# Performance work log

Measured on AMD Instinct MI355X. Metric: run time of the kernel, lower is better.

Reference implementation:

```python
import jax, jax.numpy as jnp
import numpy as np

B = 16384        # batch
N_IN = 784       # n_input_neurons
D = 64           # n_neurons_per_hidd_bank
N_LAYERS = 6     # layers of hidden banks
BANKS = 6        # banks per layer (n_hidd_banks = 36)
N_OUT = 10       # n_output_neurons
EPS = 1e-5       # BatchNorm1d eps


def setup_inputs() -> dict:
    key = jax.random.key(0)
    ks = jax.random.split(key, 8)
    x = jax.random.normal(ks[0], (B, N_IN), dtype=jnp.float32)
    gamma_in = jnp.ones((N_IN,), jnp.float32)
    beta_in = jnp.zeros((N_IN,), jnp.float32)
    # input2hidden Linear(N_IN -> D) for each of the 6 input banks (layer 0)
    W_in = jax.random.normal(ks[1], (BANKS, D, N_IN), jnp.float32) * 0.03
    b_in = jax.random.normal(ks[2], (BANKS, D), jnp.float32) * 0.03
    # per-edge gate Linear(D -> 1, no bias) and data Linear(D -> D, bias)
    # indexed [layer, source_bank, target_bank, ...]
    Wg = jax.random.normal(ks[3], (N_LAYERS - 1, BANKS, BANKS, D), jnp.float32) * 0.1
    Wd = jax.random.normal(ks[4], (N_LAYERS - 1, BANKS, BANKS, D, D), jnp.float32) * 0.1
    bd = jax.random.normal(ks[5], (N_LAYERS - 1, BANKS, BANKS, D), jnp.float32) * 0.1
    # per-bank BatchNorm1d(D) affine params, [layer, bank, D]
    gamma_h = jnp.ones((N_LAYERS, BANKS, D), jnp.float32)
    beta_h = jnp.zeros((N_LAYERS, BANKS, D), jnp.float32)
    # hidden2output Linear(D -> N_OUT, no bias) for the 6 output banks (last layer)
    W_out = jax.random.normal(ks[6], (BANKS, N_OUT, D), jnp.float32) * 0.1
    return dict(x=x, gamma_in=gamma_in, beta_in=beta_in, W_in=W_in, b_in=b_in,
                Wg=Wg, Wd=Wd, bd=bd, gamma_h=gamma_h, beta_h=beta_h, W_out=W_out)


def _bn(x, g, b):
    # training-mode BatchNorm1d: normalize over batch axis 0, biased variance
    mu = jnp.mean(x, axis=0)
    var = jnp.mean((x - mu) ** 2, axis=0)
    return g * (x - mu) * jax.lax.rsqrt(var + EPS) + b


def reference(x, gamma_in, beta_in, W_in, b_in, Wg, Wd, bd, gamma_h, beta_h, W_out):
    xb = _bn(x, gamma_in, beta_in)                                  # [B, N_IN]
    # input banks: relu(input2hidden(x)); then (as targets with no sources)
    # relu (idempotent) + BatchNorm, matching the target loop in torch
    acts = jax.nn.relu(jnp.einsum('bn,kdn->bkd', xb, W_in) + b_in)  # [B, 6, D]
    acts = _bn(jax.nn.relu(acts), gamma_h[0], beta_h[0])
    total_gate = jnp.zeros((x.shape[0], 1), x.dtype)                # sum of [B,1] gate acts
    for l in range(N_LAYERS - 1):
        # gate: hardtanh(Linear(D->1), 0, 1) per edge (s,t)
        gate = jnp.clip(jnp.einsum('bsd,std->bst', acts, Wg[l]), 0.0, 1.0)  # [B,6,6]
        # data: Linear(D->D) per edge
        data = jnp.einsum('bsd,sted->bste', acts, Wd[l]) + bd[l]            # [B,6,6,D]
        pre = jnp.einsum('bst,bste->bte', gate, data)                       # sum over sources
        total_gate = total_gate + jnp.sum(gate, axis=(1, 2))[:, None]
        acts = _bn(jax.nn.relu(pre), gamma_h[l + 1], beta_h[l + 1])         # [B,6,D]
    # output banks = last layer banks; sum of Linear(D->N_OUT, no bias)
    output = jnp.einsum('bkd,kod->bo', acts, W_out)                         # [B, N_OUT]
    return output, total_gate
```

## Files before the change

### kernel.cpp

```cpp
#include <hip/hip_runtime.h>
#include <hip/hip_bf16.h>

#define BATCH   16384
#define NIN     784
#define NH      384
#define NLAYERS 6
#define NOUT    10
#define EPS_BN  1e-5f
#define LOSCALE 2048.0f
#define LOINV   (1.0f/2048.0f)
#define NPART   128
#define PSTRIDE 1024

typedef __attribute__((ext_vector_type(8))) _Float16 f16x8;
typedef __attribute__((ext_vector_type(4))) _Float16 f16x4;
typedef __attribute__((ext_vector_type(4))) float f32x4;

__global__ __launch_bounds__(256) void stats_partial(
        const float* __restrict__ src, int C, int applyRelu,
        float* __restrict__ psum, float* __restrict__ psq) {
    int c = blockIdx.x * 256 + threadIdx.x;
    if (c >= C) return;
    int r0 = blockIdx.y * (BATCH / NPART);
    float s = 0.f, q = 0.f;
    for (int r = r0; r < r0 + BATCH / NPART; ++r) {
        float v = src[(size_t)r * C + c];
        if (applyRelu) v = fmaxf(v, 0.f);
        s += v; q += v * v;
    }
    psum[blockIdx.y * PSTRIDE + c] = s;
    psq [blockIdx.y * PSTRIDE + c] = q;
}

__global__ __launch_bounds__(256) void stats_finalize(
        const float* __restrict__ psum, const float* __restrict__ psq, int C,
        const float* __restrict__ gamma, const float* __restrict__ beta,
        float* __restrict__ a_out, float* __restrict__ c_out) {
    int c = blockIdx.x * 256 + threadIdx.x;
    if (c >= C) return;
    float s = 0.f, q = 0.f;
    for (int i = 0; i < NPART; ++i) { s += psum[i * PSTRIDE + c]; q += psq[i * PSTRIDE + c]; }
    const float invB = 1.f / (float)BATCH;
    float mu  = s * invB;
    float var = q * invB - mu * mu;
    float rs  = rsqrtf(var + EPS_BN);
    float g   = gamma[c];
    a_out[c] = g * rs;
    c_out[c] = beta[c] - g * mu * rs;
}

__global__ __launch_bounds__(256) void scale_win_hl(
        const float* __restrict__ W_in, const float* __restrict__ a,
        _Float16* __restrict__ whi, _Float16* __restrict__ wlo) {
    int i = blockIdx.x * 256 + threadIdx.x;
    if (i >= NH * NIN / 4) return;
    int n = (i * 4) % NIN;
    float4 wv = ((const float4*)W_in)[i];
    float v[4] = { wv.x * a[n], wv.y * a[n + 1], wv.z * a[n + 2], wv.w * a[n + 3] };
    f16x4 h4, l4;
    #pragma unroll
    for (int j = 0; j < 4; ++j) {
        _Float16 h = (_Float16)v[j];
        h4[j] = h;
        l4[j] = (_Float16)((v[j] - (float)h) * LOSCALE);
    }
    *(f16x4*)(whi + (size_t)i * 4) = h4;
    *(f16x4*)(wlo + (size_t)i * 4) = l4;
}

__global__ __launch_bounds__(256) void conv_hl(
        const float* __restrict__ src, _Float16* __restrict__ hi,
        _Float16* __restrict__ lo, int n4) {
    int i = blockIdx.x * 256 + threadIdx.x;
    if (i >= n4) return;
    float4 wv = ((const float4*)src)[i];
    float v[4] = { wv.x, wv.y, wv.z, wv.w };
    f16x4 h4, l4;
    #pragma unroll
    for (int j = 0; j < 4; ++j) {
        _Float16 h = (_Float16)v[j];
        h4[j] = h;
        l4[j] = (_Float16)((v[j] - (float)h) * LOSCALE);
    }
    *(f16x4*)(hi + (size_t)i * 4) = h4;
    *(f16x4*)(lo + (size_t)i * 4) = l4;
}

__global__ __launch_bounds__(256) void prep_wg(
        const float* __restrict__ Wg, _Float16* __restrict__ hi,
        _Float16* __restrict__ lo) {
    int idx = blockIdx.x * 256 + threadIdx.x;
    if (idx >= 5 * 48 * 384) return;
    int l = idx / (48 * 384);
    int r = idx % (48 * 384);
    int st = r / 384, k = r % 384;
    float v = 0.f;
    if (st < 36 && (k >> 6) == st / 6)
        v = Wg[l * 36 * 64 + st * 64 + (k & 63)];
    _Float16 h = (_Float16)v;
    hi[idx] = h;
    lo[idx] = (_Float16)((v - (float)h) * LOSCALE);
}

__global__ __launch_bounds__(256) void prep_wout(
        const float* __restrict__ W_out, _Float16* __restrict__ hi,
        _Float16* __restrict__ lo) {
    int idx = blockIdx.x * 256 + threadIdx.x;
    if (idx >= 16 * 384) return;
    int o = idx / 384, k = idx % 384;
    float v = 0.f;
    if (o < NOUT) v = W_out[((k >> 6) * NOUT + o) * 64 + (k & 63)];
    _Float16 h = (_Float16)v;
    hi[idx] = h;
    lo[idx] = (_Float16)((v - (float)h) * LOSCALE);
}

__global__ __launch_bounds__(64) void bias_in(
        const float* __restrict__ W_in, const float* __restrict__ b_in,
        const float* __restrict__ cvec, float* __restrict__ bp) {
    int j = blockIdx.x;
    int lane = threadIdx.x;
    float s = 0.f;
    for (int n = lane; n < NIN; n += 64) s += cvec[n] * W_in[j * NIN + n];
    #pragma unroll
    for (int m = 1; m < 64; m <<= 1) s += __shfl_xor(s, m, 64);
    if (lane == 0) bp[j] = b_in[j] + s;
}

__global__ __launch_bounds__(256, 2) void gemm_in_mfma(
        const float* __restrict__ X, const _Float16* __restrict__ Wphi,
        const _Float16* __restrict__ Wplo, const float* __restrict__ bp,
        float* __restrict__ pre) {
    int tid = threadIdx.x;
    int w = tid >> 6, l = tid & 63, lr = l & 15, lq = l >> 4;
    int b0 = blockIdx.x * 128 + w * 32;
    int n0 = blockIdx.y * 64;
    const float* xrow0 = X + (size_t)(b0 + lr) * NIN;
    const float* xrow1 = X + (size_t)(b0 + 16 + lr) * NIN;
    f32x4 acc[4][2], acr[4][2];
    #pragma unroll
    for (int ct = 0; ct < 4; ++ct)
        #pragma unroll
        for (int bt = 0; bt < 2; ++bt)
            #pragma unroll
            for (int r = 0; r < 4; ++r) { acc[ct][bt][r] = 0.f; acr[ct][bt][r] = 0.f; }
    for (int kc = 0; kc < 24; ++kc) {
        int k0 = kc * 32 + lq * 8;
        f16x8 ahi[2], alo[2];
        {
            float4 x0 = *(const float4*)(xrow0 + k0);
            float4 x1 = *(const float4*)(xrow0 + k0 + 4);
            float xv[8] = { x0.x, x0.y, x0.z, x0.w, x1.x, x1.y, x1.z, x1.w };
            #pragma unroll
            for (int j = 0; j < 8; ++j) {
                _Float16 h = (_Float16)xv[j];
                ahi[0][j] = h;
                alo[0][j] = (_Float16)((xv[j] - (float)h) * LOSCALE);
            }
            float4 y0 = *(const float4*)(xrow1 + k0);
            float4 y1 = *(const float4*)(xrow1 + k0 + 4);
            float yv[8] = { y0.x, y0.y, y0.z, y0.w, y1.x, y1.y, y1.z, y1.w };
            #pragma unroll
            for (int j = 0; j < 8; ++j) {
                _Float16 h = (_Float16)yv[j];
                ahi[1][j] = h;
                alo[1][j] = (_Float16)((yv[j] - (float)h) * LOSCALE);
            }
        }
        #pragma unroll
        for (int ct = 0; ct < 4; ++ct) {
            size_t off = (size_t)(n0 + ct * 16 + lr) * NIN + k0;
            f16x8 bhi = *(const f16x8*)(Wphi + off);
            f16x8 blo = *(const f16x8*)(Wplo + off);
            #pragma unroll
            for (int bt = 0; bt < 2; ++bt) {
                acc[ct][bt] = __builtin_amdgcn_mfma_f32_16x16x32_f16(ahi[bt], bhi, acc[ct][bt], 0, 0, 0);
                acr[ct][bt] = __builtin_amdgcn_mfma_f32_16x16x32_f16(ahi[bt], blo, acr[ct][bt], 0, 0, 0);
                acr[ct][bt] = __builtin_amdgcn_mfma_f32_16x16x32_f16(alo[bt], bhi, acr[ct][bt], 0, 0, 0);
            }
        }
    }
    {
        f16x8 ahi[2], alo[2];
        #pragma unroll
        for (int bt = 0; bt < 2; ++bt)
            #pragma unroll
            for (int j = 0; j < 8; ++j) { ahi[bt][j] = (_Float16)0.f; alo[bt][j] = (_Float16)0.f; }
        if (lq < 2) {
            const float* xr[2] = { xrow0, xrow1 };
            #pragma unroll
            for (int bt = 0; bt < 2; ++bt) {
                float4 x0 = *(const float4*)(xr[bt] + 768 + lq * 8);
                float4 x1 = *(const float4*)(xr[bt] + 768 + lq * 8 + 4);
                float xv[8] = { x0.x, x0.y, x0.z, x0.w, x1.x, x1.y, x1.z, x1.w };
                #pragma unroll
                for (int j = 0; j < 8; ++j) {
                    _Float16 h = (_Float16)xv[j];
                    ahi[bt][j] = h;
                    alo[bt][j] = (_Float16)((xv[j] - (float)h) * LOSCALE);
                }
            }
        }
        #pragma unroll
        for (int ct = 0; ct < 4; ++ct) {
            f16x8 bhi, blo;
            #pragma unroll
            for (int j = 0; j < 8; ++j) { bhi[j] = (_Float16)0.f; blo[j] = (_Float16)0.f; }
            if (lq < 2) {
                size_t off = (size_t)(n0 + ct * 16 + lr) * NIN + 768 + lq * 8;
                bhi = *(const f16x8*)(Wphi + off);
                blo = *(const f16x8*)(Wplo + off);
            }
            #pragma unroll
            for (int bt = 0; bt < 2; ++bt) {
                acc[ct][bt] = __builtin_amdgcn_mfma_f32_16x16x32_f16(ahi[bt], bhi, acc[ct][bt], 0, 0, 0);
                acr[ct][bt] = __builtin_amdgcn_mfma_f32_16x16x32_f16(ahi[bt], blo, acr[ct][bt], 0, 0, 0);
                acr[ct][bt] = __builtin_amdgcn_mfma_f32_16x16x32_f16(alo[bt], bhi, acr[ct][bt], 0, 0, 0);
            }
        }
    }
    #pragma unroll
    for (int ct = 0; ct < 4; ++ct) {
        int n = n0 + ct * 16 + lr;
        float bias = bp[n];
        #pragma unroll
        for (int bt = 0; bt < 2; ++bt) {
            int brow = b0 + bt * 16 + lq * 4;
            #pragma unroll
            for (int r = 0; r < 4; ++r)
                pre[(size_t)(brow + r) * NH + n] = acc[ct][bt][r] + LOINV * acr[ct][bt][r] + bias;
        }
    }
}

__global__ __launch_bounds__(256, 2) void normgate_mfma(
        const float* __restrict__ pre, const float* __restrict__ a,
        const float* __restrict__ c, const _Float16* __restrict__ WgHi,
        const _Float16* __restrict__ WgLo, _Float16* __restrict__ aHi,
        _Float16* __restrict__ aLo, float* __restrict__ gateT,
        float* __restrict__ tg, int firstLayer) {
    __shared__ float red[24][3][64];
    int tid = threadIdx.x;
    int kw = tid >> 6, l = tid & 63, lr = l & 15, lq = l >> 4;
    int b = blockIdx.x * 16 + lr;
    const float* prow = pre + (size_t)b * NH;
    f32x4 acc[3], acr[3];
    #pragma unroll
    for (int rt = 0; rt < 3; ++rt)
        #pragma unroll
        for (int r = 0; r < 4; ++r) { acc[rt][r] = 0.f; acr[rt][r] = 0.f; }
    #pragma unroll
    for (int kk = 0; kk < 3; ++kk) {
        int k0 = (kw * 3 + kk) * 32 + lq * 8;
        float4 v0 = *(const float4*)(prow + k0);
        float4 v1 = *(const float4*)(prow + k0 + 4);
        float4 a0 = *(const float4*)(a + k0);
        float4 a1 = *(const float4*)(a + k0 + 4);
        float4 c0 = *(const float4*)(c + k0);
        float4 c1 = *(const float4*)(c + k0 + 4);
        float y[8] = {
            a0.x * fmaxf(v0.x, 0.f) + c0.x, a0.y * fmaxf(v0.y, 0.f) + c0.y,
            a0.z * fmaxf(v0.z, 0.f) + c0.z, a0.w * fmaxf(v0.w, 0.f) + c0.w,
            a1.x * fmaxf(v1.x, 0.f) + c1.x, a1.y * fmaxf(v1.y, 0.f) + c1.y,
            a1.z * fmaxf(v1.z, 0.f) + c1.z, a1.w * fmaxf(v1.w, 0.f) + c1.w };
        f16x8 bhi, blo;
        #pragma unroll
        for (int j = 0; j < 8; ++j) {
            _Float16 h = (_Float16)y[j];
            bhi[j] = h;
            blo[j] = (_Float16)((y[j] - (float)h) * LOSCALE);
        }
        *(f16x8*)(aHi + (size_t)b * NH + k0) = bhi;
        *(f16x8*)(aLo + (size_t)b * NH + k0) = blo;
        #pragma unroll
        for (int rt = 0; rt < 3; ++rt) {
            size_t off = (size_t)(rt * 16 + lr) * NH + k0;
            f16x8 whi = *(const f16x8*)(WgHi + off);
            f16x8 wlo = *(const f16x8*)(WgLo + off);
            acc[rt] = __builtin_amdgcn_mfma_f32_16x16x32_f16(whi, bhi, acc[rt], 0, 0, 0);
            acr[rt] = __builtin_amdgcn_mfma_f32_16x16x32_f16(whi, blo, acr[rt], 0, 0, 0);
            acr[rt] = __builtin_amdgcn_mfma_f32_16x16x32_f16(wlo, bhi, acr[rt], 0, 0, 0);
        }
    }
    if (kw > 0) {
        #pragma unroll
        for (int rt = 0; rt < 3; ++rt)
            #pragma unroll
            for (int r = 0; r < 4; ++r) {
                red[rt * 4 + r][kw - 1][l]      = acc[rt][r];
                red[12 + rt * 4 + r][kw - 1][l] = acr[rt][r];
            }
    }
    __syncthreads();
    if (kw == 0) {
        #pragma unroll
        for (int rt = 0; rt < 3; ++rt)
            #pragma unroll
            for (int r = 0; r < 4; ++r) {
                #pragma unroll
                for (int wv = 0; wv < 3; ++wv) {
                    acc[rt][r] += red[rt * 4 + r][wv][l];
                    acr[rt][r] += red[12 + rt * 4 + r][wv][l];
                }
            }
        float gsum = 0.f;
        #pragma unroll
        for (int rt = 0; rt < 3; ++rt)
            #pragma unroll
            for (int r = 0; r < 4; ++r) {
                int st = rt * 16 + lq * 4 + r;
                if (st < 36) {
                    float p = acc[rt][r] + LOINV * acr[rt][r];
                    float g = fminf(fmaxf(p, 0.f), 1.f);
                    gateT[(size_t)st * BATCH + b] = g;
                    gsum += g;
                }
            }
        gsum += __shfl_xor(gsum, 16, 64);
        gsum += __shfl_xor(gsum, 32, 64);
        if (lq == 0) tg[b] = (firstLayer ? 0.f : tg[b]) + gsum;
    }
}

__global__ __launch_bounds__(256, 2) void layer_data_mfma(
        const _Float16* __restrict__ aHi, const _Float16* __restrict__ aLo,
        const float* __restrict__ gateT, const _Float16* __restrict__ Wdhi,
        const _Float16* __restrict__ Wdlo, const float* __restrict__ bd_l,
        float* __restrict__ pre) {
    int tid = threadIdx.x;
    int w = tid >> 6, l = tid & 63, lr = l & 15, lq = l >> 4;
    int b0 = blockIdx.x * 32;
    int t0 = blockIdx.y * 3;
    int e0 = w * 16;
    f32x4 acc[3][2];
    #pragma unroll
    for (int t = 0; t < 3; ++t)
        #pragma unroll
        for (int ct = 0; ct < 2; ++ct)
            #pragma unroll
            for (int r = 0; r < 4; ++r) acc[t][ct][r] = 0.f;
    #pragma unroll 1
    for (int s = 0; s < 6; ++s) {
        f16x8 bhi[2][2], blo[2][2];
        #pragma unroll
        for (int ct = 0; ct < 2; ++ct) {
            size_t arow = (size_t)(b0 + ct * 16 + lr) * NH + s * 64 + lq * 8;
            #pragma unroll
            for (int ks = 0; ks < 2; ++ks) {
                bhi[ct][ks] = *(const f16x8*)(aHi + arow + ks * 32);
                blo[ct][ks] = *(const f16x8*)(aLo + arow + ks * 32);
            }
        }
        #pragma unroll
        for (int tt = 0; tt < 3; ++tt) {
            int t = t0 + tt;
            float g[2];
            #pragma unroll
            for (int ct = 0; ct < 2; ++ct)
                g[ct] = gateT[(size_t)(s * 6 + t) * BATCH + b0 + ct * 16 + lr];
            size_t wb = ((size_t)(s * 6 + t) * 64 + e0 + lr) * 64 + lq * 8;
            f16x8 ah0 = *(const f16x8*)(Wdhi + wb);
            f16x8 ah1 = *(const f16x8*)(Wdhi + wb + 32);
            f16x8 al0 = *(const f16x8*)(Wdlo + wb);
            f16x8 al1 = *(const f16x8*)(Wdlo + wb + 32);
            float bdv[4];
            #pragma unroll
            for (int r = 0; r < 4; ++r)
                bdv[r] = bd_l[(s * 6 + t) * 64 + e0 + lq * 4 + r];
            #pragma unroll
            for (int ct = 0; ct < 2; ++ct) {
                f32x4 ph, pc;
                #pragma unroll
                for (int r = 0; r < 4; ++r) { ph[r] = 0.f; pc[r] = 0.f; }
                ph = __builtin_amdgcn_mfma_f32_16x16x32_f16(ah0, bhi[ct][0], ph, 0, 0, 0);
                ph = __builtin_amdgcn_mfma_f32_16x16x32_f16(ah1, bhi[ct][1], ph, 0, 0, 0);
                pc = __builtin_amdgcn_mfma_f32_16x16x32_f16(ah0, blo[ct][0], pc, 0, 0, 0);
                pc = __builtin_amdgcn_mfma_f32_16x16x32_f16(ah1, blo[ct][1], pc, 0, 0, 0);
                pc = __builtin_amdgcn_mfma_f32_16x16x32_f16(al0, bhi[ct][0], pc, 0, 0, 0);
                pc = __builtin_amdgcn_mfma_f32_16x16x32_f16(al1, bhi[ct][1], pc, 0, 0, 0);
                #pragma unroll
                for (int r = 0; r < 4; ++r)
                    acc[tt][ct][r] += g[ct] * (ph[r] + LOINV * pc[r] + bdv[r]);
            }
        }
    }
    #pragma unroll
    for (int tt = 0; tt < 3; ++tt)
        #pragma unroll
        for (int ct = 0; ct < 2; ++ct)
            #pragma unroll
            for (int r = 0; r < 4; ++r)
                pre[(size_t)(b0 + ct * 16 + lr) * NH + (t0 + tt) * 64 + e0 + lq * 4 + r]
                    = acc[tt][ct][r];
}

__global__ __launch_bounds__(256, 2) void normout_mfma(
        const float* __restrict__ pre, const float* __restrict__ a,
        const float* __restrict__ c, const _Float16* __restrict__ OutHi,
        const _Float16* __restrict__ OutLo, const float* __restrict__ tg,
        float* __restrict__ dout) {
    __shared__ float red[8][3][64];
    int tid = threadIdx.x;
    int kw = tid >> 6, l = tid & 63, lr = l & 15, lq = l >> 4;
    int b = blockIdx.x * 16 + lr;
    const float* prow = pre + (size_t)b * NH;
    f32x4 acc, acr;
    #pragma unroll
    for (int r = 0; r < 4; ++r) { acc[r] = 0.f; acr[r] = 0.f; }
    #pragma unroll
    for (int kk = 0; kk < 3; ++kk) {
        int k0 = (kw * 3 + kk) * 32 + lq * 8;
        float4 v0 = *(const float4*)(prow + k0);
        float4 v1 = *(const float4*)(prow + k0 + 4);
        float4 a0 = *(const float4*)(a + k0);
        float4 a1 = *(const float4*)(a + k0 + 4);
        float4 c0 = *(const float4*)(c + k0);
        float4 c1 = *(const float4*)(c + k0 + 4);
        float y[8] = {
            a0.x * fmaxf(v0.x, 0.f) + c0.x, a0.y * fmaxf(v0.y, 0.f) + c0.y,
            a0.z * fmaxf(v0.z, 0.f) + c0.z, a0.w * fmaxf(v0.w, 0.f) + c0.w,
            a1.x * fmaxf(v1.x, 0.f) + c1.x, a1.y * fmaxf(v1.y, 0.f) + c1.y,
            a1.z * fmaxf(v1.z, 0.f) + c1.z, a1.w * fmaxf(v1.w, 0.f) + c1.w };
        f16x8 bhi, blo;
        #pragma unroll
        for (int j = 0; j < 8; ++j) {
            _Float16 h = (_Float16)y[j];
            bhi[j] = h;
            blo[j] = (_Float16)((y[j] - (float)h) * LOSCALE);
        }
        size_t off = (size_t)lr * NH + k0;
        f16x8 whi = *(const f16x8*)(OutHi + off);
        f16x8 wlo = *(const f16x8*)(OutLo + off);
        acc = __builtin_amdgcn_mfma_f32_16x16x32_f16(whi, bhi, acc, 0, 0, 0);
        acr = __builtin_amdgcn_mfma_f32_16x16x32_f16(whi, blo, acr, 0, 0, 0);
        acr = __builtin_amdgcn_mfma_f32_16x16x32_f16(wlo, bhi, acr, 0, 0, 0);
    }
    if (kw > 0) {
        #pragma unroll
        for (int r = 0; r < 4; ++r) {
            red[r][kw - 1][l]     = acc[r];
            red[4 + r][kw - 1][l] = acr[r];
        }
    }
    __syncthreads();
    if (kw == 0) {
        #pragma unroll
        for (int r = 0; r < 4; ++r)
            #pragma unroll
            for (int wv = 0; wv < 3; ++wv) {
                acc[r] += red[r][wv][l];
                acr[r] += red[4 + r][wv][l];
            }
        #pragma unroll
        for (int r = 0; r < 4; ++r) {
            int o = lq * 4 + r;
            if (o < NOUT)
                dout[(size_t)b * NOUT + o] = acc[r] + LOINV * acr[r];
        }
        if (lq == 0) dout[(size_t)BATCH * NOUT + b] = tg[b];
    }
}

extern "C" void kernel_launch(void* const* d_in, const int* in_sizes, int n_in,
                              void* d_out, int out_size, void* d_ws, size_t ws_size,
                              hipStream_t stream) {
    const float* x        = (const float*)d_in[0];
    const float* gamma_in = (const float*)d_in[1];
    const float* beta_in  = (const float*)d_in[2];
    const float* W_in     = (const float*)d_in[3];
    const float* b_in     = (const float*)d_in[4];
    const float* Wg       = (const float*)d_in[5];
    const float* Wd       = (const float*)d_in[6];
    const float* bd       = (const float*)d_in[7];
    const float* gamma_h  = (const float*)d_in[8];
    const float* beta_h   = (const float*)d_in[9];
    const float* W_out    = (const float*)d_in[10];
    float* dout = (float*)d_out;
    float* ws = (float*)d_ws;

    float* psum  = ws;
    float* psq   = ws + 131072;
    float* avec  = ws + 262144;
    float* cvec  = ws + 263168;
    float* bp    = ws + 264192;
    float* pre   = ws + 265216;
    _Float16* actsHi = (_Float16*)(ws + 6556672);
    _Float16* actsLo = (_Float16*)(ws + 9702400);
    float* gateT = ws + 12848128;
    float* tg    = ws + 13437952;
    _Float16* WpHi = (_Float16*)(ws + 13454336);
    _Float16* WpLo = (_Float16*)(ws + 13604864);
    _Float16* WdHiAll = (_Float16*)(ws + 13755392);
    _Float16* WdLoAll = (_Float16*)(ws + 14124032);
    _Float16* WgHiAll = (_Float16*)(ws + 14492672);
    _Float16* WgLoAll = (_Float16*)(ws + 14538752);
    _Float16* OutHi   = (_Float16*)(ws + 14584832);
    _Float16* OutLo   = (_Float16*)(ws + 14587904);

    dim3 blk(256);

    stats_partial<<<dim3(4, NPART), blk, 0, stream>>>(x, NIN, 0, psum, psq);
    stats_finalize<<<dim3(4), blk, 0, stream>>>(psum, psq, NIN, gamma_in, beta_in, avec, cvec);
    scale_win_hl<<<dim3((NH * NIN / 4 + 255) / 256), blk, 0, stream>>>(W_in, avec, WpHi, WpLo);
    bias_in<<<dim3(NH), dim3(64), 0, stream>>>(W_in, b_in, cvec, bp);
    conv_hl<<<dim3((5 * 36 * 4096 / 4 + 255) / 256), blk, 0, stream>>>(
            Wd, WdHiAll, WdLoAll, 5 * 36 * 4096 / 4);
    prep_wg<<<dim3((5 * 48 * 384 + 255) / 256), blk, 0, stream>>>(Wg, WgHiAll, WgLoAll);
    prep_wout<<<dim3((16 * 384 + 255) / 256), blk, 0, stream>>>(W_out, OutHi, OutLo);

    gemm_in_mfma<<<dim3(BATCH / 128, 6), blk, 0, stream>>>(x, WpHi, WpLo, bp, pre);

    for (int j = 0; j < NLAYERS; ++j) {
        stats_partial<<<dim3(2, NPART), blk, 0, stream>>>(pre, NH, 1, psum, psq);
        stats_finalize<<<dim3(2), blk, 0, stream>>>(psum, psq, NH,
                gamma_h + j * NH, beta_h + j * NH, avec, cvec);
        if (j < NLAYERS - 1) {
            int l = j;
            normgate_mfma<<<dim3(BATCH / 16), blk, 0, stream>>>(
                    pre, avec, cvec, WgHiAll + (size_t)l * 48 * 384,
                    WgLoAll + (size_t)l * 48 * 384, actsHi, actsLo, gateT, tg, l == 0);
            layer_data_mfma<<<dim3(BATCH / 32, 2), blk, 0, stream>>>(
                    actsHi, actsLo, gateT, WdHiAll + (size_t)l * 36 * 4096,
                    WdLoAll + (size_t)l * 36 * 4096, bd + (size_t)l * 36 * 64, pre);
        } else {
            normout_mfma<<<dim3(BATCH / 16), blk, 0, stream>>>(
                    pre, avec, cvec, OutHi, OutLo, tg, dout);
        }
    }
}
```

Baseline: 642.2 us.

## Split input GEMM K-dimension across waves with shared-memory reduction

```diff
diff --git a/kernel.cpp b/kernel.cpp
--- a/kernel.cpp
+++ b/kernel.cpp
@@ -131,9 +131,10 @@
         const float* __restrict__ X, const _Float16* __restrict__ Wphi,
         const _Float16* __restrict__ Wplo, const float* __restrict__ bp,
         float* __restrict__ pre) {
+    __shared__ float red[32][3][64];
     int tid = threadIdx.x;
-    int w = tid >> 6, l = tid & 63, lr = l & 15, lq = l >> 4;
-    int b0 = blockIdx.x * 128 + w * 32;
+    int kw = tid >> 6, l = tid & 63, lr = l & 15, lq = l >> 4;
+    int b0 = blockIdx.x * 32;
     int n0 = blockIdx.y * 64;
     const float* xrow0 = X + (size_t)(b0 + lr) * NIN;
     const float* xrow1 = X + (size_t)(b0 + 16 + lr) * NIN;
@@ -144,8 +145,8 @@
         for (int bt = 0; bt < 2; ++bt)
             #pragma unroll
             for (int r = 0; r < 4; ++r) { acc[ct][bt][r] = 0.f; acr[ct][bt][r] = 0.f; }
-    for (int kc = 0; kc < 24; ++kc) {
-        int k0 = kc * 32 + lq * 8;
+    for (int kk = 0; kk < 6; ++kk) {
+        int k0 = (kw * 6 + kk) * 32 + lq * 8;
         f16x8 ahi[2], alo[2];
         {
             float4 x0 = *(const float4*)(xrow0 + k0);
@@ -180,7 +181,7 @@
             }
         }
     }
-    {
+    if (kw == 3) {
         f16x8 ahi[2], alo[2];
         #pragma unroll
         for (int bt = 0; bt < 2; ++bt)
@@ -219,16 +220,34 @@
             }
         }
     }
-    #pragma unroll
-    for (int ct = 0; ct < 4; ++ct) {
-        int n = n0 + ct * 16 + lr;
-        float bias = bp[n];
-        #pragma unroll
-        for (int bt = 0; bt < 2; ++bt) {
-            int brow = b0 + bt * 16 + lq * 4;
-            #pragma unroll
-            for (int r = 0; r < 4; ++r)
-                pre[(size_t)(brow + r) * NH + n] = acc[ct][bt][r] + LOINV * acr[ct][bt][r] + bias;
+    if (kw > 0) {
+        #pragma unroll
+        for (int ct = 0; ct < 4; ++ct)
+            #pragma unroll
+            for (int bt = 0; bt < 2; ++bt)
+                #pragma unroll
+                for (int r = 0; r < 4; ++r)
+                    red[ct * 8 + bt * 4 + r][kw - 1][l]
+                        = acc[ct][bt][r] + LOINV * acr[ct][bt][r];
+    }
+    __syncthreads();
+    if (kw == 0) {
+        #pragma unroll
+        for (int ct = 0; ct < 4; ++ct) {
+            int n = n0 + ct * 16 + lr;
+            float bias = bp[n];
+            #pragma unroll
+            for (int bt = 0; bt < 2; ++bt) {
+                int brow = b0 + bt * 16 + lq * 4;
+                #pragma unroll
+                for (int r = 0; r < 4; ++r) {
+                    float v = acc[ct][bt][r] + LOINV * acr[ct][bt][r];
+                    #pragma unroll
+                    for (int wv = 0; wv < 3; ++wv)
+                        v += red[ct * 8 + bt * 4 + r][wv][l];
+                    pre[(size_t)(brow + r) * NH + n] = v + bias;
+                }
+            }
         }
     }
 }
@@ -339,7 +358,6 @@
         for (int ct = 0; ct < 2; ++ct)
             #pragma unroll
             for (int r = 0; r < 4; ++r) acc[t][ct][r] = 0.f;
-    #pragma unroll 1
     for (int s = 0; s < 6; ++s) {
         f16x8 bhi[2][2], blo[2][2];
         #pragma unroll
@@ -508,7 +526,7 @@
     prep_wg<<<dim3((5 * 48 * 384 + 255) / 256), blk, 0, stream>>>(Wg, WgHiAll, WgLoAll);
     prep_wout<<<dim3((16 * 384 + 255) / 256), blk, 0, stream>>>(W_out, OutHi, OutLo);
 
-    gemm_in_mfma<<<dim3(BATCH / 128, 6), blk, 0, stream>>>(x, WpHi, WpLo, bp, pre);
+    gemm_in_mfma<<<dim3(BATCH / 32, 6), blk, 0, stream>>>(x, WpHi, WpLo, bp, pre);
 
     for (int j = 0; j < NLAYERS; ++j) {
         stats_partial<<<dim3(2, NPART), blk, 0, stream>>>(pre, NH, 1, psum, psq);
```

Measured after the change: 773.1 us. 20.4% more time.
